# Kernel tuning notes

Hardware: AMD Instinct MI355X
Metric: run time of the kernel (lower is better)

## Reference

```python
import jax, jax.numpy as jnp
import numpy as np

D_MODEL = 1024
N_HEADS = 16
D_V = D_MODEL // N_HEADS  # 64; o_proj maps d_model -> d_v (quirk of the source)
B, S = 4, 2048


def setup_inputs() -> dict:
    key = jax.random.key(0)
    ks = jax.random.split(key, 5)
    scale = 1.0 / np.sqrt(D_MODEL)
    return {
        "in_features": jax.random.normal(ks[0], (B, S, D_MODEL), dtype=jnp.float32),
        "Wq": jax.random.normal(ks[1], (D_MODEL, D_MODEL), dtype=jnp.float32) * scale,
        "Wk": jax.random.normal(ks[2], (D_MODEL, D_MODEL), dtype=jnp.float32) * scale,
        "Wv": jax.random.normal(ks[3], (D_MODEL, D_MODEL), dtype=jnp.float32) * scale,
        "Wo": jax.random.normal(ks[4], (D_V, D_MODEL), dtype=jnp.float32) * scale,
    }


def reference(in_features, Wq, Wk, Wv, Wo):
    # Linear(in, out): y = x @ W^T, no bias. NOTE: source never splits heads;
    # attention runs single-head over the full d_model dims.
    Q = jnp.einsum('bsd,ed->bse', in_features, Wq)  # [B,S,D]
    K = jnp.einsum('bsd,ed->bse', in_features, Wk)
    V = jnp.einsum('bsd,ed->bse', in_features, Wv)

    scores = jnp.einsum('bqd,bkd->bqk', Q, K)       # [B,S,S]
    causal = jnp.tril(jnp.ones((S, S), dtype=bool))  # True = keep
    # source applies -inf mask BEFORE scaling (equivalent result)
    scores = jnp.where(causal[None, :, :], scores, -jnp.inf)
    scores = scores / jnp.sqrt(jnp.float32(D_MODEL))  # K.size(-1) == d_model
    attn = jax.nn.softmax(scores, axis=-1)
    ctx = jnp.einsum('bqk,bkd->bqd', attn, V)        # [B,S,D]
    return jnp.einsum('bsd,vd->bsv', ctx, Wo)        # [B,S,D_V]
```

## Files before the change

kernel.cpp:

```cpp
#include <hip/hip_runtime.h>
#include <math.h>

typedef unsigned short u16;
typedef unsigned int u32;
typedef __attribute__((ext_vector_type(8))) short short8;
typedef __attribute__((ext_vector_type(4))) short short4v;
typedef __attribute__((ext_vector_type(4))) float f32x4;

#define BB 4
#define SS 2048
#define DD 1024
#define DV 64
#define NYU 1152
#define BS (BB * SS)
#define SCALE (1.0f / 32.0f)
#define NTILE 136
#define NSLOT (BB * NTILE)

__device__ __forceinline__ u16 f2bf(float f) {
    u32 u = __builtin_bit_cast(u32, f);
    u32 r = u + 0x7fffu + ((u >> 16) & 1u);
    return (u16)(r >> 16);
}
__device__ __forceinline__ float bf2f(u16 b) {
    return __builtin_bit_cast(float, (u32)b << 16);
}

__global__ __launch_bounds__(256) void prep(const float* __restrict__ x,
                                            const float* __restrict__ Wq,
                                            const float* __restrict__ Wk,
                                            const float* __restrict__ Wv,
                                            const float* __restrict__ Wo,
                                            u16* __restrict__ x16,
                                            u16* __restrict__ Wqt,
                                            u16* __restrict__ Wkt,
                                            u16* __restrict__ Wvt,
                                            u16* __restrict__ Wo16) {
    __shared__ u16 t[64 * 72];
    const int b = blockIdx.x;
    const int tid = threadIdx.x;
    if (b < 768) {
        const int sel = b >> 8;
        const float* src = (sel == 0) ? Wq : (sel == 1) ? Wk : Wv;
        u16* dst = (sel == 0) ? Wqt : (sel == 1) ? Wkt : Wvt;
        const int rem = b & 255;
        const int e0 = (rem >> 4) * 64, d0 = (rem & 15) * 64;
        const int g = tid >> 6, lane = tid & 63;
        for (int r = g; r < 64; r += 4)
            t[r * 72 + lane] = f2bf(src[(size_t)(e0 + r) * DD + d0 + lane]);
        __syncthreads();
        for (int r = g; r < 64; r += 4)
            dst[(size_t)(d0 + r) * DD + e0 + lane] = t[lane * 72 + r];
    } else if (b < 784) {
#pragma unroll
        for (int j = 0; j < 4; ++j) {
            int i = (b - 768) * 1024 + j * 256 + tid;
            f32x4 v = ((const f32x4*)Wo)[i];
            short4v o;
            o.x = (short)f2bf(v.x); o.y = (short)f2bf(v.y);
            o.z = (short)f2bf(v.z); o.w = (short)f2bf(v.w);
            ((short4v*)Wo16)[i] = o;
        }
    } else {
        int i = (b - 784) * 256 + tid;
        f32x4 v = ((const f32x4*)x)[i];
        short4v o;
        o.x = (short)f2bf(v.x); o.y = (short)f2bf(v.y);
        o.z = (short)f2bf(v.z); o.w = (short)f2bf(v.w);
        ((short4v*)x16)[i] = o;
    }
}

__global__ __launch_bounds__(256) void gt_wvo(const u16* __restrict__ Wkt,
                                              const u16* __restrict__ Wqt,
                                              const u16* __restrict__ Wo16,
                                              const u16* __restrict__ Wvt,
                                              u16* __restrict__ GpartH,
                                              u16* __restrict__ WvoPartH) {
    const int b = blockIdx.x;
    const u16 *A, *B;
    u16* C;
    int m0, n0;
    if (b < 1024) {
        const int z = b >> 8, t = b & 255;
        A = Wkt + z * 256;
        B = Wqt + z * 256;
        C = GpartH + (size_t)z * DD * DD;
        m0 = (t >> 4) * 64;
        n0 = (t & 15) * 64;
    } else {
        const int bb = b - 1024;
        const int kc = bb >> 4, t = bb & 15;
        A = Wo16 + kc * 256;
        B = Wvt + kc * 256;
        C = WvoPartH + (size_t)kc * DV * DD;
        m0 = 0;
        n0 = t * 64;
    }

    __shared__ u16 As[2][64 * 32];
    __shared__ u16 Bs[2][64 * 32];

    const int tid = threadIdx.x;
    const int w = tid >> 6, lane = tid & 63;
    const int wm = w >> 1, wn = w & 1;
    const int lrow = lane >> 2;
    const int lcolsw = (((lane & 3) ^ ((lrow >> 1) & 3)) << 3);
    const int m16 = lane & 15;
    const int rdo = (((lane >> 4) ^ ((m16 >> 1) & 3)) << 3);

    f32x4 acc[2][2];
#pragma unroll
    for (int i = 0; i < 2; ++i)
#pragma unroll
        for (int j = 0; j < 2; ++j) acc[i][j] = (f32x4){0.f, 0.f, 0.f, 0.f};

    auto stage = [&](int t_, int bufi) {
        const int k0 = t_ * 32;
        {
            const u16* g = A + (size_t)(m0 + w * 16 + lrow) * DD + k0 + lcolsw;
            __builtin_amdgcn_global_load_lds(
                (const __attribute__((address_space(1))) void*)g,
                (__attribute__((address_space(3))) void*)(&As[bufi][w * 512]), 16, 0, 0);
        }
        {
            const u16* g = B + (size_t)(n0 + w * 16 + lrow) * DD + k0 + lcolsw;
            __builtin_amdgcn_global_load_lds(
                (const __attribute__((address_space(1))) void*)g,
                (__attribute__((address_space(3))) void*)(&Bs[bufi][w * 512]), 16, 0, 0);
        }
    };

    stage(0, 0);
    asm volatile("s_waitcnt vmcnt(0)" ::: "memory");
    __syncthreads();

    int cur = 0;
    for (int t_ = 0; t_ < 8; ++t_) {
        if (t_ + 1 < 8) stage(t_ + 1, cur ^ 1);

        short8 a[2], bb[2];
#pragma unroll
        for (int i = 0; i < 2; ++i)
            a[i] = *(const short8*)&As[cur][(wm * 32 + i * 16 + m16) * 32 + rdo];
#pragma unroll
        for (int j = 0; j < 2; ++j)
            bb[j] = *(const short8*)&Bs[cur][(wn * 32 + j * 16 + m16) * 32 + rdo];
#pragma unroll
        for (int i = 0; i < 2; ++i)
#pragma unroll
            for (int j = 0; j < 2; ++j)
                acc[i][j] = __builtin_amdgcn_mfma_f32_16x16x32_bf16(a[i], bb[j], acc[i][j], 0, 0, 0);

        if (t_ + 1 < 8) {
            asm volatile("s_waitcnt vmcnt(0)" ::: "memory");
            __syncthreads();
        }
        cur ^= 1;
    }

    const int crow0 = m0 + wm * 32 + (lane >> 4) * 4;
    const int ccol0 = n0 + wn * 32 + m16;
#pragma unroll
    for (int i = 0; i < 2; ++i)
#pragma unroll
        for (int j = 0; j < 2; ++j)
#pragma unroll
            for (int r = 0; r < 4; ++r)
                C[(size_t)(crow0 + i * 16 + r) * DD + ccol0 + j * 16] = f2bf(acc[i][j][r]);
}

__global__ __launch_bounds__(256) void reduce_all(const u16* __restrict__ GpartH,
                                                  const u16* __restrict__ WvoPartH,
                                                  u16* __restrict__ Wall2) {
    const int bx = blockIdx.x;
    const int e0 = threadIdx.x * 4;
    float s0 = 0.f, s1 = 0.f, s2 = 0.f, s3 = 0.f;
#pragma unroll
    for (int kc = 0; kc < 4; ++kc) {
        const u16* src = (bx < 1024)
                             ? &GpartH[(size_t)kc * DD * DD + (size_t)bx * DD + e0]
                             : &WvoPartH[(size_t)kc * DV * DD + (size_t)(bx - 1024) * DD + e0];
        short4v v = *(const short4v*)src;
        s0 += bf2f((u16)v.x); s1 += bf2f((u16)v.y);
        s2 += bf2f((u16)v.z); s3 += bf2f((u16)v.w);
    }
    short4v ov;
    ov.x = (short)f2bf(s0); ov.y = (short)f2bf(s1);
    ov.z = (short)f2bf(s2); ov.w = (short)f2bf(s3);
    *(short4v*)&Wall2[(size_t)bx * DD + e0] = ov;
}

__global__ __launch_bounds__(512) void yu_gemm(const u16* __restrict__ x16,
                                               const u16* __restrict__ Wall2,
                                               u16* __restrict__ YU,
                                               u16* __restrict__ Ut) {
    const int b = blockIdx.x;
    const int r = b & 7, q = b >> 3;
    const int m0 = (r * 8 + q / 9) * 128;
    const int n0 = (q % 9) * 128;

    __shared__ u16 As[2][128 * 32];
    __shared__ u16 Bs[2][128 * 32];

    const int tid = threadIdx.x;
    const int w = tid >> 6, lane = tid & 63;
    const int wm = w >> 2, wn = w & 3;
    const int lrow = lane >> 2;
    const int lcolsw = (((lane & 3) ^ ((lrow >> 1) & 3)) << 3);
    const int m16 = lane & 15;
    const int rdo = (((lane >> 4) ^ ((m16 >> 1) & 3)) << 3);

    f32x4 acc[4][2];
#pragma unroll
    for (int i = 0; i < 4; ++i)
#pragma unroll
        for (int j = 0; j < 2; ++j) acc[i][j] = (f32x4){0.f, 0.f, 0.f, 0.f};

    auto stage = [&](int t, int bufi) {
        const int k0 = t * 32;
        {
            const u16* g = x16 + (size_t)(m0 + w * 16 + lrow) * DD + k0 + lcolsw;
            __builtin_amdgcn_global_load_lds(
                (const __attribute__((address_space(1))) void*)g,
                (__attribute__((address_space(3))) void*)(&As[bufi][w * 512]), 16, 0, 0);
        }
        {
            const u16* g = Wall2 + (size_t)(n0 + w * 16 + lrow) * DD + k0 + lcolsw;
            __builtin_amdgcn_global_load_lds(
                (const __attribute__((address_space(1))) void*)g,
                (__attribute__((address_space(3))) void*)(&Bs[bufi][w * 512]), 16, 0, 0);
        }
    };

    stage(0, 0);
    asm volatile("s_waitcnt vmcnt(0)" ::: "memory");
    __syncthreads();

    int cur = 0;
    for (int t = 0; t < 32; ++t) {
        if (t + 1 < 32) stage(t + 1, cur ^ 1);

        short8 a[4], bb[2];
#pragma unroll
        for (int i = 0; i < 4; ++i)
            a[i] = *(const short8*)&As[cur][(wm * 64 + i * 16 + m16) * 32 + rdo];
#pragma unroll
        for (int j = 0; j < 2; ++j)
            bb[j] = *(const short8*)&Bs[cur][(wn * 32 + j * 16 + m16) * 32 + rdo];
#pragma unroll
        for (int i = 0; i < 4; ++i)
#pragma unroll
            for (int j = 0; j < 2; ++j)
                acc[i][j] = __builtin_amdgcn_mfma_f32_16x16x32_bf16(a[i], bb[j], acc[i][j], 0, 0, 0);

        if (t + 1 < 32) {
            asm volatile("s_waitcnt vmcnt(0)" ::: "memory");
            __syncthreads();
        }
        cur ^= 1;
    }

    const int crow0 = m0 + wm * 64 + (lane >> 4) * 4;
    const int ccol0 = n0 + wn * 32 + m16;
#pragma unroll
    for (int i = 0; i < 4; ++i)
#pragma unroll
        for (int j = 0; j < 2; ++j)
#pragma unroll
            for (int r = 0; r < 4; ++r) {
                const float v = acc[i][j][r];
                YU[(size_t)(crow0 + i * 16 + r) * NYU + ccol0 + j * 16] = f2bf(v);
                if (n0 == 1024 && wn < 2)
                    Ut[(size_t)(ccol0 + j * 16 - 1024) * BS + crow0 + i * 16 + r] = f2bf(v);
            }
}

__global__ __launch_bounds__(512) void scores_pv(const u16* __restrict__ YU,
                                                 const u16* __restrict__ x16,
                                                 const u16* __restrict__ Ut,
                                                 float* __restrict__ Opart,
                                                 float* __restrict__ Lpart) {
    const int b = blockIdx.x;
    const int r8 = b & 7;
    const int z = r8 >> 1;
    const int t = 2 * (b >> 3) + (r8 & 1);
    int y = (int)((sqrtf(8.f * t + 1.f) - 1.f) * 0.5f);
    while ((y + 1) * (y + 2) / 2 <= t) ++y;
    while (y * (y + 1) / 2 > t) --y;
    const int m0 = y * 128;
    const int n0 = (t - y * (y + 1) / 2) * 128;
    const int tglob = z * NTILE + t;

    const u16* A = YU + (size_t)z * SS * NYU;
    const u16* B = x16 + (size_t)z * SS * DD;

    __shared__ union ShU {
        struct { u16 As[2][128 * 32]; u16 Bs[2][128 * 32]; } s;
        u16 Ps[128 * 136];
    } sh;

    const int tid = threadIdx.x;
    const int w = tid >> 6, lane = tid & 63;
    const int wm = w >> 2, wn = w & 3;
    const int lrow = lane >> 2;
    const int lcolsw = (((lane & 3) ^ ((lrow >> 1) & 3)) << 3);
    const int m16 = lane & 15;
    const int kh = (lane >> 4) * 8;
    const int rdo = (((lane >> 4) ^ ((m16 >> 1) & 3)) << 3);

    f32x4 acc[4][2];
#pragma unroll
    for (int i = 0; i < 4; ++i)
#pragma unroll
        for (int j = 0; j < 2; ++j) acc[i][j] = (f32x4){0.f, 0.f, 0.f, 0.f};

    auto stage = [&](int tt, int bufi) {
        const int k0 = tt * 32;
        {
            const u16* g = A + (size_t)(m0 + w * 16 + lrow) * NYU + k0 + lcolsw;
            __builtin_amdgcn_global_load_lds(
                (const __attribute__((address_space(1))) void*)g,
                (__attribute__((address_space(3))) void*)(&sh.s.As[bufi][w * 512]), 16, 0, 0);
        }
        {
            const u16* g = B + (size_t)(n0 + w * 16 + lrow) * DD + k0 + lcolsw;
            __builtin_amdgcn_global_load_lds(
                (const __attribute__((address_space(1))) void*)g,
                (__attribute__((address_space(3))) void*)(&sh.s.Bs[bufi][w * 512]), 16, 0, 0);
        }
    };

    stage(0, 0);
    asm volatile("s_waitcnt vmcnt(0)" ::: "memory");
    __syncthreads();

    int cur = 0;
    for (int tt = 0; tt < 32; ++tt) {
        if (tt + 1 < 32) stage(tt + 1, cur ^ 1);

        short8 a[4], bb[2];
#pragma unroll
        for (int i = 0; i < 4; ++i)
            a[i] = *(const short8*)&sh.s.As[cur][(wm * 64 + i * 16 + m16) * 32 + rdo];
#pragma unroll
        for (int j = 0; j < 2; ++j)
            bb[j] = *(const short8*)&sh.s.Bs[cur][(wn * 32 + j * 16 + m16) * 32 + rdo];
#pragma unroll
        for (int i = 0; i < 4; ++i)
#pragma unroll
            for (int j = 0; j < 2; ++j)
                acc[i][j] = __builtin_amdgcn_mfma_f32_16x16x32_bf16(a[i], bb[j], acc[i][j], 0, 0, 0);

        if (tt + 1 < 32) {
            asm volatile("s_waitcnt vmcnt(0)" ::: "memory");
            __syncthreads();
        }
        cur ^= 1;
    }
    __syncthreads();

    const int rl0 = wm * 64 + (lane >> 4) * 4;
    const int cl0 = wn * 32 + m16;
#pragma unroll
    for (int i = 0; i < 4; ++i)
#pragma unroll
        for (int j = 0; j < 2; ++j)
#pragma unroll
            for (int r = 0; r < 4; ++r) {
                const int rl = rl0 + i * 16 + r;
                const int cl = cl0 + j * 16;
                float p = __expf(acc[i][j][r] * SCALE);
                sh.Ps[rl * 136 + cl] = (n0 + cl <= m0 + rl) ? f2bf(p) : (u16)0;
            }
    __syncthreads();

    short8 ones8;
#pragma unroll
    for (int e = 0; e < 8; ++e) ones8[e] = (short)0x3F80;

    const u16* Utz = Ut + (size_t)z * SS + n0;
    f32x4 accO[4], accL;
    accL = (f32x4){0.f, 0.f, 0.f, 0.f};
#pragma unroll
    for (int j = 0; j < 4; ++j) accO[j] = (f32x4){0.f, 0.f, 0.f, 0.f};
#pragma unroll
    for (int ks = 0; ks < 4; ++ks) {
        const int k0 = ks * 32;
        short8 a = *(const short8*)&sh.Ps[(w * 16 + m16) * 136 + k0 + kh];
        short8 bb[4];
#pragma unroll
        for (int j = 0; j < 4; ++j)
            bb[j] = *(const short8*)&Utz[(size_t)(j * 16 + m16) * BS + k0 + kh];
#pragma unroll
        for (int j = 0; j < 4; ++j)
            accO[j] = __builtin_amdgcn_mfma_f32_16x16x32_bf16(a, bb[j], accO[j], 0, 0, 0);
        accL = __builtin_amdgcn_mfma_f32_16x16x32_bf16(a, ones8, accL, 0, 0, 0);
    }

    float* Op = Opart + (size_t)tglob * (128 * 64);
    float* Lp = Lpart + (size_t)tglob * 128;
    const int lr0 = w * 16 + (lane >> 4) * 4;
#pragma unroll
    for (int j = 0; j < 4; ++j)
#pragma unroll
        for (int r = 0; r < 4; ++r)
            Op[(size_t)(lr0 + r) * DV + j * 16 + m16] = accO[j][r];
    if (m16 == 0)
#pragma unroll
        for (int r = 0; r < 4; ++r)
            Lp[lr0 + r] = accL[r];
}

__global__ __launch_bounds__(256) void normalize(float* __restrict__ out,
                                                 const float* __restrict__ Opart,
                                                 const float* __restrict__ Lpart) {
    const int i = blockIdx.x * 256 + threadIdx.x;
    const int row = i >> 4;
    const int z = row >> 11, s = row & 2047;
    const int y = s >> 7, lr = s & 127;
    const int base = z * NTILE + y * (y + 1) / 2;
    const int nc = y + 1;
    const int col4 = (i & 15) * 4;

    f32x4 acc = (f32x4){0.f, 0.f, 0.f, 0.f};
    float L = 0.f;
    for (int c = 0; c < nc; ++c) {
        const int slot = base + c;
        acc += *(const f32x4*)&Opart[(size_t)slot * (128 * 64) + (size_t)lr * 64 + col4];
        L += Lpart[(size_t)slot * 128 + lr];
    }
    const float inv = 1.f / L;
    acc.x *= inv; acc.y *= inv; acc.z *= inv; acc.w *= inv;
    ((f32x4*)out)[i] = acc;
}

extern "C" void kernel_launch(void* const* d_in, const int* in_sizes, int n_in,
                              void* d_out, int out_size, void* d_ws, size_t ws_size,
                              hipStream_t stream) {
    const float* x  = (const float*)d_in[0];
    const float* Wq = (const float*)d_in[1];
    const float* Wk = (const float*)d_in[2];
    const float* Wv = (const float*)d_in[3];
    const float* Wo = (const float*)d_in[4];
    float* out = (float*)d_out;

    u16* x16   = (u16*)d_ws;
    u16* Wqt   = x16 + (size_t)BB * SS * DD;
    u16* Wkt   = Wqt + (size_t)DD * DD;
    u16* Wvt   = Wkt + (size_t)DD * DD;
    u16* Wo16  = Wvt + (size_t)DD * DD;
    u16* Wall2 = Wo16 + (size_t)DV * DD;
    u16* YU    = Wall2 + (size_t)NYU * DD;
    u16* Ut    = YU + (size_t)BB * SS * NYU;
    float* Opart = (float*)(Ut + (size_t)DV * BS);
    float* Lpart = Opart + (size_t)NSLOT * 128 * DV;
    u16* GpartH   = YU;
    u16* WvoPartH = GpartH + (size_t)4 * DD * DD;

    prep<<<dim3(8976), 256, 0, stream>>>(x, Wq, Wk, Wv, Wo, x16, Wqt, Wkt, Wvt, Wo16);

    gt_wvo<<<dim3(1088), 256, 0, stream>>>(Wkt, Wqt, Wo16, Wvt, GpartH, WvoPartH);

    reduce_all<<<dim3(1088), 256, 0, stream>>>(GpartH, WvoPartH, Wall2);

    yu_gemm<<<dim3(576), 512, 0, stream>>>(x16, Wall2, YU, Ut);

    scores_pv<<<dim3(544), 512, 0, stream>>>(YU, x16, Ut, Opart, Lpart);

    normalize<<<dim3(out_size / 4 / 256), 256, 0, stream>>>(out, Opart, Lpart);
}
```

Baseline: 178.0 us.

## Overlap x bf16 cast with weight-product GEMM and store partial outputs as bf16

The fp32-to-bf16 cast of the activations moves out of the prep kernel and into the Wk^T·Wq / Wvo GEMM launch as extra blocks, so it runs concurrently with that compute-bound work. The prep kernel now only handles the weights. Per-tile partial attention outputs are stored in bf16 rather than fp32, halving the write and readback traffic between scores_pv and normalize. This costs some precision in the partial sums before normalization.

```diff
diff --git a/kernel.cpp b/kernel.cpp
--- a/kernel.cpp
+++ b/kernel.cpp
@@ -26,16 +26,14 @@
     return __builtin_bit_cast(float, (u32)b << 16);
 }
 
-__global__ __launch_bounds__(256) void prep(const float* __restrict__ x,
-                                            const float* __restrict__ Wq,
-                                            const float* __restrict__ Wk,
-                                            const float* __restrict__ Wv,
-                                            const float* __restrict__ Wo,
-                                            u16* __restrict__ x16,
-                                            u16* __restrict__ Wqt,
-                                            u16* __restrict__ Wkt,
-                                            u16* __restrict__ Wvt,
-                                            u16* __restrict__ Wo16) {
+__global__ __launch_bounds__(256) void prep_w(const float* __restrict__ Wq,
+                                              const float* __restrict__ Wk,
+                                              const float* __restrict__ Wv,
+                                              const float* __restrict__ Wo,
+                                              u16* __restrict__ Wqt,
+                                              u16* __restrict__ Wkt,
+                                              u16* __restrict__ Wvt,
+                                              u16* __restrict__ Wo16) {
     __shared__ u16 t[64 * 72];
     const int b = blockIdx.x;
     const int tid = threadIdx.x;
@@ -51,7 +49,7 @@
         __syncthreads();
         for (int r = g; r < 64; r += 4)
             dst[(size_t)(d0 + r) * DD + e0 + lane] = t[lane * 72 + r];
-    } else if (b < 784) {
+    } else {
 #pragma unroll
         for (int j = 0; j < 4; ++j) {
             int i = (b - 768) * 1024 + j * 256 + tid;
@@ -61,23 +59,29 @@
             o.z = (short)f2bf(v.z); o.w = (short)f2bf(v.w);
             ((short4v*)Wo16)[i] = o;
         }
-    } else {
-        int i = (b - 784) * 256 + tid;
+    }
+}
+
+__global__ __launch_bounds__(256) void gtwvo_cast(const u16* __restrict__ Wkt,
+                                                  const u16* __restrict__ Wqt,
+                                                  const u16* __restrict__ Wo16,
+                                                  const u16* __restrict__ Wvt,
+                                                  const float* __restrict__ x,
+                                                  u16* __restrict__ x16,
+                                                  u16* __restrict__ GpartH,
+                                                  u16* __restrict__ WvoPartH) {
+    const int b = blockIdx.x;
+    const int tid = threadIdx.x;
+    if (b >= 1088) {
+        int i = (b - 1088) * 256 + tid;
         f32x4 v = ((const f32x4*)x)[i];
         short4v o;
         o.x = (short)f2bf(v.x); o.y = (short)f2bf(v.y);
         o.z = (short)f2bf(v.z); o.w = (short)f2bf(v.w);
         ((short4v*)x16)[i] = o;
-    }
-}
-
-__global__ __launch_bounds__(256) void gt_wvo(const u16* __restrict__ Wkt,
-                                              const u16* __restrict__ Wqt,
-                                              const u16* __restrict__ Wo16,
-                                              const u16* __restrict__ Wvt,
-                                              u16* __restrict__ GpartH,
-                                              u16* __restrict__ WvoPartH) {
-    const int b = blockIdx.x;
+        return;
+    }
+
     const u16 *A, *B;
     u16* C;
     int m0, n0;
@@ -101,7 +105,6 @@
     __shared__ u16 As[2][64 * 32];
     __shared__ u16 Bs[2][64 * 32];
 
-    const int tid = threadIdx.x;
     const int w = tid >> 6, lane = tid & 63;
     const int wm = w >> 1, wn = w & 1;
     const int lrow = lane >> 2;
@@ -279,7 +282,7 @@
 __global__ __launch_bounds__(512) void scores_pv(const u16* __restrict__ YU,
                                                  const u16* __restrict__ x16,
                                                  const u16* __restrict__ Ut,
-                                                 float* __restrict__ Opart,
+                                                 u16* __restrict__ Opart,
                                                  float* __restrict__ Lpart) {
     const int b = blockIdx.x;
     const int r8 = b & 7;
@@ -398,14 +401,14 @@
         accL = __builtin_amdgcn_mfma_f32_16x16x32_bf16(a, ones8, accL, 0, 0, 0);
     }
 
-    float* Op = Opart + (size_t)tglob * (128 * 64);
+    u16* Op = Opart + (size_t)tglob * (128 * 64);
     float* Lp = Lpart + (size_t)tglob * 128;
     const int lr0 = w * 16 + (lane >> 4) * 4;
 #pragma unroll
     for (int j = 0; j < 4; ++j)
 #pragma unroll
         for (int r = 0; r < 4; ++r)
-            Op[(size_t)(lr0 + r) * DV + j * 16 + m16] = accO[j][r];
+            Op[(size_t)(lr0 + r) * DV + j * 16 + m16] = f2bf(accO[j][r]);
     if (m16 == 0)
 #pragma unroll
         for (int r = 0; r < 4; ++r)
@@ -413,7 +416,7 @@
 }
 
 __global__ __launch_bounds__(256) void normalize(float* __restrict__ out,
-                                                 const float* __restrict__ Opart,
+                                                 const u16* __restrict__ Opart,
                                                  const float* __restrict__ Lpart) {
     const int i = blockIdx.x * 256 + threadIdx.x;
     const int row = i >> 4;
@@ -427,7 +430,9 @@
     float L = 0.f;
     for (int c = 0; c < nc; ++c) {
         const int slot = base + c;
-        acc += *(const f32x4*)&Opart[(size_t)slot * (128 * 64) + (size_t)lr * 64 + col4];
+        short4v v = *(const short4v*)&Opart[(size_t)slot * (128 * 64) + (size_t)lr * 64 + col4];
+        acc.x += bf2f((u16)v.x); acc.y += bf2f((u16)v.y);
+        acc.z += bf2f((u16)v.z); acc.w += bf2f((u16)v.w);
         L += Lpart[(size_t)slot * 128 + lr];
     }
     const float inv = 1.f / L;
@@ -453,14 +458,15 @@
     u16* Wall2 = Wo16 + (size_t)DV * DD;
     u16* YU    = Wall2 + (size_t)NYU * DD;
     u16* Ut    = YU + (size_t)BB * SS * NYU;
-    float* Opart = (float*)(Ut + (size_t)DV * BS);
-    float* Lpart = Opart + (size_t)NSLOT * 128 * DV;
+    u16* Opart = Ut + (size_t)DV * BS;
+    float* Lpart = (float*)(Opart + (size_t)NSLOT * 128 * DV);
     u16* GpartH   = YU;
     u16* WvoPartH = GpartH + (size_t)4 * DD * DD;
 
-    prep<<<dim3(8976), 256, 0, stream>>>(x, Wq, Wk, Wv, Wo, x16, Wqt, Wkt, Wvt, Wo16);
-
-    gt_wvo<<<dim3(1088), 256, 0, stream>>>(Wkt, Wqt, Wo16, Wvt, GpartH, WvoPartH);
+    prep_w<<<dim3(784), 256, 0, stream>>>(Wq, Wk, Wv, Wo, Wqt, Wkt, Wvt, Wo16);
+
+    gtwvo_cast<<<dim3(9280), 256, 0, stream>>>(Wkt, Wqt, Wo16, Wvt, x, x16,
+                                               GpartH, WvoPartH);
 
     reduce_all<<<dim3(1088), 256, 0, stream>>>(GpartH, WvoPartH, Wall2);
 
```

New measurement: 175.9 us. No clear change (-1.2%).
